# Optimization experiments

Measured on AMD Instinct MI355X. Metric: run time of the kernel, lower is better.

## Reference

```python
import jax, jax.numpy as jnp
import numpy as np

EMBED_DIM = 1024
NUM_HEADS = 16
HEAD_DIM = EMBED_DIM // NUM_HEADS
B, T = 4, 2048


def setup_inputs() -> dict:
    key = jax.random.key(0)
    ks = jax.random.split(key, 5)
    s = 1.0 / np.sqrt(EMBED_DIM)
    x = jax.random.normal(ks[0], (B, T, EMBED_DIM), dtype=jnp.float32)
    attention_mask = jnp.ones((B, 1, 1, T), dtype=jnp.int32)
    # torch Linear weights: qkv (3E, E), out (E, E); store transposed for x @ W
    W_qkv = jax.random.uniform(ks[1], (EMBED_DIM, 3 * EMBED_DIM), jnp.float32, -s, s)
    b_qkv = jax.random.uniform(ks[2], (3 * EMBED_DIM,), jnp.float32, -s, s)
    W_out = jax.random.uniform(ks[3], (EMBED_DIM, EMBED_DIM), jnp.float32, -s, s)
    b_out = jax.random.uniform(ks[4], (EMBED_DIM,), jnp.float32, -s, s)
    return {"x": x, "attention_mask": attention_mask,
            "W_qkv": W_qkv, "b_qkv": b_qkv, "W_out": W_out, "b_out": b_out}


def reference(x, attention_mask, W_qkv, b_qkv, W_out, b_out):
    Bq, Tq, E = x.shape
    qkv = x @ W_qkv + b_qkv                              # [B,T,3E]
    qkv = qkv.reshape(Bq, Tq, 3, NUM_HEADS, HEAD_DIM)
    qkv = jnp.transpose(qkv, (2, 0, 3, 1, 4))            # [3,B,H,T,d]
    q, k, v = qkv[0], qkv[1], qkv[2]
    scores = jnp.einsum('bhqd,bhkd->bhqk', q, k) / jnp.sqrt(
        jnp.asarray(HEAD_DIM, x.dtype))                  # [B,H,T,T]
    scores = jnp.where(attention_mask == 0, jnp.asarray(-jnp.inf, x.dtype), scores)
    attn = jax.nn.softmax(scores, axis=-1)
    ctx = jnp.einsum('bhqk,bhkd->bhqd', attn, v)         # [B,H,T,d]
    ctx = jnp.transpose(ctx, (0, 2, 1, 3)).reshape(Bq, Tq, E)
    return ctx @ W_out + b_out
```

## Files before the change

kernel.cpp:

```cpp
#include <hip/hip_runtime.h>
#include <hip/hip_bf16.h>
#include <stdint.h>


typedef __attribute__((ext_vector_type(8))) short short8;
typedef __attribute__((ext_vector_type(4))) float f32x4;
typedef __attribute__((ext_vector_type(16))) float f32x16;
typedef __attribute__((ext_vector_type(4))) unsigned short ushort4_t;
typedef __attribute__((ext_vector_type(8))) unsigned short ushort8_t;

#define SEQ 2048
#define EDIM 1024
#define QSCALE 0.18033688011112042f

__device__ __forceinline__ unsigned short f2bf(float x) {
  union { float f; uint32_t u; } v; v.f = x;
  uint32_t r = v.u + 0x7fffu + ((v.u >> 16) & 1u);
  return (unsigned short)(r >> 16);
}

__device__ __forceinline__ uint32_t cvtpk(float lo, float hi) {
  uint32_t r;
  asm("v_cvt_pk_bf16_f32 %0, %1, %2" : "=v"(r) : "v"(lo), "v"(hi));
  return r;
}

__device__ __forceinline__ float exp2_raw(float x) {
  float r;
  asm("v_exp_f32 %0, %1" : "=v"(r) : "v"(x));
  return r;
}

__device__ __forceinline__ void gload_lds16(const void* g, void* l) {
  typedef __attribute__((address_space(1))) const unsigned int gu32;
  typedef __attribute__((address_space(3))) unsigned int lu32;
  __builtin_amdgcn_global_load_lds((gu32*)g, (lu32*)l, 16, 0, 0);
}

__global__ void k_prep(const float* __restrict__ x,
                       unsigned short* __restrict__ xb,
                       const float* __restrict__ Wq,
                       unsigned short* __restrict__ wqt,
                       const float* __restrict__ Wo,
                       unsigned short* __restrict__ wot) {
  __shared__ float tile[32][33];
  const int id = blockIdx.x;
  if (id < 4096) {
    const int i = id * 256 + threadIdx.x;
    const float4* p = ((const float4*)x) + (size_t)i * 2;
    float4 a = p[0], b = p[1];
    ushort8_t v;
    v[0] = f2bf(a.x); v[1] = f2bf(a.y); v[2] = f2bf(a.z); v[3] = f2bf(a.w);
    v[4] = f2bf(b.x); v[5] = f2bf(b.y); v[6] = f2bf(b.z); v[7] = f2bf(b.w);
    ((ushort8_t*)xb)[i] = v;
    return;
  }
  const float* W;
  unsigned short* Wt;
  int N, bx, by;
  if (id < 7168) { W = Wq; Wt = wqt; N = 3072; bx = (id - 4096) % 96; by = (id - 4096) / 96; }
  else           { W = Wo; Wt = wot; N = 1024; bx = (id - 7168) % 32; by = (id - 7168) / 32; }
  const int K = 1024;
  const int c0 = bx * 32, r0 = by * 32;
  const int tx = threadIdx.x & 31, ty = threadIdx.x >> 5;
#pragma unroll
  for (int i = 0; i < 4; ++i) {
    int r = ty + i * 8;
    tile[r][tx] = W[(size_t)(r0 + r) * N + c0 + tx];
  }
  __syncthreads();
#pragma unroll
  for (int i = 0; i < 4; ++i) {
    int r = ty + i * 8;
    Wt[(size_t)(c0 + r) * K + r0 + tx] = f2bf(tile[tx][r]);
  }
}

template <int EPI, int NBX>
__global__ __launch_bounds__(256, 2) void k_gemm(
    const unsigned short* __restrict__ A, const unsigned short* __restrict__ Bt,
    const float* __restrict__ bias, unsigned short* __restrict__ Qo,
    unsigned short* __restrict__ Ko, unsigned short* __restrict__ VTo,
    float* __restrict__ Out) {
  __shared__ unsigned short As[128 * 32];
  __shared__ unsigned short Bs[128 * 32];
  const int tid = threadIdx.x;
  const int lane = tid & 63, wid = tid >> 6;
  const int wr = wid >> 1, wc = wid & 1;
  const int g = lane >> 4, r = lane & 15;
  const int lid = blockIdx.y * NBX + blockIdx.x;
  const int total = NBX * gridDim.y;
  const int id = (lid & 7) * (total >> 3) + (lid >> 3);
  const int m0 = (id / NBX) * 128, n0 = (id % NBX) * 128;

  f32x4 zero4 = {0.f, 0.f, 0.f, 0.f};
  f32x4 acc[4][4];
#pragma unroll
  for (int mi = 0; mi < 4; ++mi)
#pragma unroll
    for (int ni = 0; ni < 4; ++ni) acc[mi][ni] = zero4;

  for (int kt = 0; kt < 1024; kt += 32) {
#pragma unroll
    for (int i = 0; i < 2; ++i) {
      int seg = i * 256 + tid;
      int row = seg >> 2, sl = seg & 3;
      gload_lds16(A + (size_t)(m0 + row) * 1024 + kt + sl * 8,
                  (char*)As + (i * 256 + wid * 64) * 16);
      gload_lds16(Bt + (size_t)(n0 + row) * 1024 + kt + sl * 8,
                  (char*)Bs + (i * 256 + wid * 64) * 16);
    }
    __syncthreads();
    short8 af[4], bf[4];
#pragma unroll
    for (int mi = 0; mi < 4; ++mi)
      af[mi] = *(const short8*)&As[(wr * 64 + mi * 16 + r) * 32 + g * 8];
#pragma unroll
    for (int ni = 0; ni < 4; ++ni)
      bf[ni] = *(const short8*)&Bs[(wc * 64 + ni * 16 + r) * 32 + g * 8];
#pragma unroll
    for (int mi = 0; mi < 4; ++mi)
#pragma unroll
      for (int ni = 0; ni < 4; ++ni)
        acc[mi][ni] = __builtin_amdgcn_mfma_f32_16x16x32_bf16(
            af[mi], bf[ni], acc[mi][ni], 0, 0, 0);
    __syncthreads();
  }

#pragma unroll
  for (int mi = 0; mi < 4; ++mi) {
#pragma unroll
    for (int ni = 0; ni < 4; ++ni) {
      const int n = n0 + wc * 64 + ni * 16 + r;
      const float bv = bias[n];
      const int mbase = m0 + wr * 64 + mi * 16 + g * 4;
      if (EPI == 0) {
        const int sec = n >> 10, e = n & 1023, h = e >> 6, dd = e & 63;
        const int b = mbase >> 11, t = mbase & 2047;
        if (sec == 2) {
          ushort4_t pk;
#pragma unroll
          for (int j = 0; j < 4; ++j) pk[j] = f2bf(acc[mi][ni][j] + bv);
          *(ushort4_t*)&VTo[(((size_t)b * 16 + h) * 64 + dd) * 2048 + t] = pk;
        } else {
          unsigned short* dst = (sec == 0) ? Qo : Ko;
          const float scl = (sec == 0) ? QSCALE : 1.0f;
#pragma unroll
          for (int j = 0; j < 4; ++j)
            dst[(((size_t)b * 16 + h) * 2048 + t + j) * 64 + dd] =
                f2bf((acc[mi][ni][j] + bv) * scl);
        }
      } else {
#pragma unroll
        for (int j = 0; j < 4; ++j)
          Out[(size_t)(mbase + j) * 1024 + n] = acc[mi][ni][j] + bv;
      }
    }
  }
}

__global__ __launch_bounds__(256, 4) void k_attn(
    const unsigned short* __restrict__ Qg, const unsigned short* __restrict__ Kg,
    const unsigned short* __restrict__ VTg, const int* __restrict__ maskp,
    unsigned short* __restrict__ ctx) {
  __shared__ unsigned short Ks[3][64 * 64];
  __shared__ unsigned short Vs[3][64 * 64];
  const int tid = threadIdx.x, lane = tid & 63, wid = tid >> 6;
  const int q = lane & 31, hi = lane >> 5;
  const int id = blockIdx.x;
  const int slot = id >> 3;
  const int bh = (id & 7) * 8 + (slot >> 4);
  const int b = bh >> 4, h = bh & 15;
  const int q0 = (slot & 15) * 128 + wid * 32;
  const int qr = q0 + q;

  const unsigned short* Qb = Qg + (size_t)bh * SEQ * 64;
  const unsigned short* Kb = Kg + (size_t)bh * SEQ * 64;
  const unsigned short* Vb = VTg + (size_t)bh * 64 * SEQ;
  const int* mb = maskp + b * SEQ;

  const int r0_ = tid >> 3, sl0_ = (tid & 7) ^ (r0_ & 7);
  const int r1_ = (256 + tid) >> 3, sl1_ = ((256 + tid) & 7) ^ (r1_ & 7);
  const unsigned short* kp0 = Kb + r0_ * 64 + sl0_ * 8;
  const unsigned short* kp1 = Kb + r1_ * 64 + sl1_ * 8;
  const unsigned short* vp0 = Vb + (size_t)r0_ * SEQ + sl0_ * 8;
  const unsigned short* vp1 = Vb + (size_t)r1_ * SEQ + sl1_ * 8;
  char* kbase = (char*)Ks[0] + wid * 1024;
  char* vbase = (char*)Vs[0] + wid * 1024;

  auto STAGE = [&](int bo) {
    gload_lds16(kp0, kbase + bo);
    gload_lds16(kp1, kbase + bo + 4096);
    gload_lds16(vp0, vbase + bo);
    gload_lds16(vp1, vbase + bo + 4096);
    kp0 += 64 * 64; kp1 += 64 * 64;
    vp0 += 64; vp1 += 64;
  };

  short8 qf[4];
#pragma unroll
  for (int ds = 0; ds < 4; ++ds)
    qf[ds] = *(const short8*)&Qb[(size_t)qr * 64 + ds * 16 + hi * 8];

  short8 onesf;
#pragma unroll
  for (int j = 0; j < 8; ++j) onesf[j] = (short)0x3F80;

  f32x16 z16 = {0.f,0.f,0.f,0.f,0.f,0.f,0.f,0.f,0.f,0.f,0.f,0.f,0.f,0.f,0.f,0.f};
  f32x16 o0 = z16, o1 = z16;
  f32x16 osum = z16;
  short8 pfp[4];
#pragma unroll
  for (int j = 0; j < 4; ++j) pfp[j] = onesf;
  const int kb4 = hi * 4;

  STAGE(0);
  const int* mptr = mb + lane;
  int mv = mptr[0];
  mptr += 64;
  int cur = 0, nxt = 1, prv = 2;

  for (int t = 0; t < 32; ++t) {
    __syncthreads();
    int mvn = 1;
    if (t < 31) {
      STAGE(nxt * 8192);
      mvn = mptr[0];
      mptr += 64;
    }
    const unsigned long long bits = __ballot(mv != 0);
    mv = mvn;

    const char* KsB = (const char*)Ks[0] + cur * 8192;
    const char* VsP = (const char*)Vs[0] + prv * 8192;

    f32x16 c0 = z16, c1 = z16;
    __builtin_amdgcn_s_setprio(1);
#pragma unroll
    for (int ds = 0; ds < 4; ++ds) {
      const int sl = ds * 2 + hi;
      short8 ka0 = *(const short8*)(KsB + q * 128 + ((sl ^ (q & 7)) * 16));
      short8 ka1 = *(const short8*)(KsB + (32 + q) * 128 + ((sl ^ (q & 7)) * 16));
      c0 = __builtin_amdgcn_mfma_f32_32x32x16_bf16(ka0, qf[ds], c0, 0, 0, 0);
      c1 = __builtin_amdgcn_mfma_f32_32x32x16_bf16(ka1, qf[ds], c1, 0, 0, 0);
    }

    if (t > 0) {
#pragma unroll
      for (int ks = 0; ks < 4; ++ks) {
        const int sl = ks * 2 + hi;
        short8 va0 = *(const short8*)(VsP + q * 128 + ((sl ^ (q & 7)) * 16));
        short8 va1 = *(const short8*)(VsP + (32 + q) * 128 + ((sl ^ (q & 7)) * 16));
        o0 = __builtin_amdgcn_mfma_f32_32x32x16_bf16(va0, pfp[ks], o0, 0, 0, 0);
        o1 = __builtin_amdgcn_mfma_f32_32x32x16_bf16(va1, pfp[ks], o1, 0, 0, 0);
        osum = __builtin_amdgcn_mfma_f32_32x32x16_bf16(onesf, pfp[ks], osum,
                                                       0, 0, 0);
      }
    }
    __builtin_amdgcn_s_setprio(0);

#pragma unroll
    for (int i = 0; i < 16; ++i) {
      c0[i] = exp2_raw(c0[i]);
      c1[i] = exp2_raw(c1[i]);
    }
    if (bits != ~0ull) {
#pragma unroll
      for (int i = 0; i < 16; ++i) {
        const int k0 = (i & 3) + 8 * (i >> 2) + kb4;
        if (!((bits >> k0) & 1)) c0[i] = 0.f;
        if (!((bits >> (k0 + 32)) & 1)) c1[i] = 0.f;
      }
    }

#pragma unroll
    for (int sub = 0; sub < 2; ++sub) {
      uint32_t w[8];
#pragma unroll
      for (int j = 0; j < 8; ++j)
        w[j] = sub ? cvtpk(c1[2 * j], c1[2 * j + 1])
                   : cvtpk(c0[2 * j], c0[2 * j + 1]);
      asm("v_permlane32_swap_b32 %0, %1" : "+v"(w[0]), "+v"(w[2]));
      asm("v_permlane32_swap_b32 %0, %1" : "+v"(w[1]), "+v"(w[3]));
      asm("v_permlane32_swap_b32 %0, %1" : "+v"(w[4]), "+v"(w[6]));
      asm("v_permlane32_swap_b32 %0, %1" : "+v"(w[5]), "+v"(w[7]));
      union { uint32_t u[4]; short8 s; } ua, ub;
      ua.u[0] = w[0]; ua.u[1] = w[1]; ua.u[2] = w[2]; ua.u[3] = w[3];
      ub.u[0] = w[4]; ub.u[1] = w[5]; ub.u[2] = w[6]; ub.u[3] = w[7];
      pfp[sub * 2] = ua.s;
      pfp[sub * 2 + 1] = ub.s;
    }

    prv = cur; cur = nxt; nxt = (nxt == 2) ? 0 : nxt + 1;
  }

  {
    const char* VsP = (const char*)Vs[0] + prv * 8192;
    __builtin_amdgcn_s_setprio(1);
#pragma unroll
    for (int ks = 0; ks < 4; ++ks) {
      const int sl = ks * 2 + hi;
      short8 va0 = *(const short8*)(VsP + q * 128 + ((sl ^ (q & 7)) * 16));
      short8 va1 = *(const short8*)(VsP + (32 + q) * 128 + ((sl ^ (q & 7)) * 16));
      o0 = __builtin_amdgcn_mfma_f32_32x32x16_bf16(va0, pfp[ks], o0, 0, 0, 0);
      o1 = __builtin_amdgcn_mfma_f32_32x32x16_bf16(va1, pfp[ks], o1, 0, 0, 0);
      osum = __builtin_amdgcn_mfma_f32_32x32x16_bf16(onesf, pfp[ks], osum,
                                                     0, 0, 0);
    }
    __builtin_amdgcn_s_setprio(0);
  }

  const float inv = 1.f / osum[0];
#pragma unroll
  for (int ns = 0; ns < 2; ++ns) {
#pragma unroll
    for (int g_ = 0; g_ < 4; ++g_) {
      ushort4_t v4;
#pragma unroll
      for (int e = 0; e < 4; ++e) {
        const float val = (ns ? o1[g_ * 4 + e] : o0[g_ * 4 + e]) * inv;
        v4[e] = f2bf(val);
      }
      *(ushort4_t*)&ctx[((size_t)b * SEQ + qr) * 1024 + h * 64 + ns * 32 +
                        g_ * 8 + hi * 4] = v4;
    }
  }
}

extern "C" void kernel_launch(void* const* d_in, const int* in_sizes, int n_in,
                              void* d_out, int out_size, void* d_ws,
                              size_t ws_size, hipStream_t stream) {
  const float* x = (const float*)d_in[0];
  const int* mask = (const int*)d_in[1];
  const float* Wqkv = (const float*)d_in[2];
  const float* bqkv = (const float*)d_in[3];
  const float* Wout = (const float*)d_in[4];
  const float* bout = (const float*)d_in[5];
  float* out = (float*)d_out;

  unsigned short* ws = (unsigned short*)d_ws;
  unsigned short* xb = ws;
  unsigned short* wqt = ws + 8388608;
  unsigned short* wot = ws + 11534336;
  unsigned short* Q = ws + 12582912;
  unsigned short* K = ws + 20971520;
  unsigned short* VT = ws + 29360128;
  unsigned short* ctx = xb;

  k_prep<<<8192, 256, 0, stream>>>(x, xb, Wqkv, wqt, Wout, wot);
  k_gemm<0, 24><<<dim3(24, 64), 256, 0, stream>>>(xb, wqt, bqkv, Q, K, VT,
                                                  nullptr);
  k_attn<<<1024, 256, 0, stream>>>(Q, K, VT, mask, ctx);
  k_gemm<1, 8><<<dim3(8, 64), 256, 0, stream>>>(ctx, wot, bout, nullptr,
                                                nullptr, nullptr, out);
}
```

Baseline: 202.5 us.

## Split attention KV tiles across wave pairs and reduce partial outputs in LDS

Each attention block now covers 64 queries with four waves arranged as two query groups times two key halves, so the grid doubles to 2048 blocks. Each wave computes scores for 32 of the 64 keys in a tile and accumulates a partial PV product and row sum. The partials are combined through LDS at the end. The software pipeline drops from three buffers with a one-step deferred PV to two buffers with the PV done in the same step, which cuts LDS use and lengthens the dependency chain inside each iteration. This trades more K/V tile loads per query and an extra reduction for higher parallelism and occupancy.

After: 251.1 us. 1.24x slower.

```diff
diff --git a/kernel.cpp b/kernel.cpp
--- a/kernel.cpp
+++ b/kernel.cpp
@@ -163,15 +163,16 @@
     const unsigned short* __restrict__ Qg, const unsigned short* __restrict__ Kg,
     const unsigned short* __restrict__ VTg, const int* __restrict__ maskp,
     unsigned short* __restrict__ ctx) {
-  __shared__ unsigned short Ks[3][64 * 64];
-  __shared__ unsigned short Vs[3][64 * 64];
+  __shared__ unsigned short Ks[2][64 * 64];
+  __shared__ unsigned short Vs[2][64 * 64];
   const int tid = threadIdx.x, lane = tid & 63, wid = tid >> 6;
+  const int wq = wid >> 1, wk = wid & 1;
   const int q = lane & 31, hi = lane >> 5;
   const int id = blockIdx.x;
   const int slot = id >> 3;
-  const int bh = (id & 7) * 8 + (slot >> 4);
+  const int bh = (id & 7) * 8 + (slot >> 5);
   const int b = bh >> 4, h = bh & 15;
-  const int q0 = (slot & 15) * 128 + wid * 32;
+  const int q0 = (slot & 31) * 64 + wq * 32;
   const int qr = q0 + q;
 
   const unsigned short* Qb = Qg + (size_t)bh * SEQ * 64;
@@ -188,7 +189,8 @@
   char* kbase = (char*)Ks[0] + wid * 1024;
   char* vbase = (char*)Vs[0] + wid * 1024;
 
-  auto STAGE = [&](int bo) {
+  auto STAGE = [&](int buf) {
+    const int bo = buf * 8192;
     gload_lds16(kp0, kbase + bo);
     gload_lds16(kp1, kbase + bo + 4096);
     gload_lds16(vp0, vbase + bo);
@@ -209,77 +211,54 @@
   f32x16 z16 = {0.f,0.f,0.f,0.f,0.f,0.f,0.f,0.f,0.f,0.f,0.f,0.f,0.f,0.f,0.f,0.f};
   f32x16 o0 = z16, o1 = z16;
   f32x16 osum = z16;
-  short8 pfp[4];
-#pragma unroll
-  for (int j = 0; j < 4; ++j) pfp[j] = onesf;
   const int kb4 = hi * 4;
 
   STAGE(0);
   const int* mptr = mb + lane;
   int mv = mptr[0];
   mptr += 64;
-  int cur = 0, nxt = 1, prv = 2;
 
   for (int t = 0; t < 32; ++t) {
+    const int cur = t & 1;
     __syncthreads();
     int mvn = 1;
     if (t < 31) {
-      STAGE(nxt * 8192);
+      STAGE(cur ^ 1);
       mvn = mptr[0];
       mptr += 64;
     }
     const unsigned long long bits = __ballot(mv != 0);
     mv = mvn;
 
-    const char* KsB = (const char*)Ks[0] + cur * 8192;
-    const char* VsP = (const char*)Vs[0] + prv * 8192;
-
-    f32x16 c0 = z16, c1 = z16;
+    const char* KsB = (const char*)Ks[cur];
+    const char* VsB = (const char*)Vs[cur];
+
+    f32x16 c0 = z16;
     __builtin_amdgcn_s_setprio(1);
 #pragma unroll
     for (int ds = 0; ds < 4; ++ds) {
       const int sl = ds * 2 + hi;
-      short8 ka0 = *(const short8*)(KsB + q * 128 + ((sl ^ (q & 7)) * 16));
-      short8 ka1 = *(const short8*)(KsB + (32 + q) * 128 + ((sl ^ (q & 7)) * 16));
-      c0 = __builtin_amdgcn_mfma_f32_32x32x16_bf16(ka0, qf[ds], c0, 0, 0, 0);
-      c1 = __builtin_amdgcn_mfma_f32_32x32x16_bf16(ka1, qf[ds], c1, 0, 0, 0);
-    }
-
-    if (t > 0) {
-#pragma unroll
-      for (int ks = 0; ks < 4; ++ks) {
-        const int sl = ks * 2 + hi;
-        short8 va0 = *(const short8*)(VsP + q * 128 + ((sl ^ (q & 7)) * 16));
-        short8 va1 = *(const short8*)(VsP + (32 + q) * 128 + ((sl ^ (q & 7)) * 16));
-        o0 = __builtin_amdgcn_mfma_f32_32x32x16_bf16(va0, pfp[ks], o0, 0, 0, 0);
-        o1 = __builtin_amdgcn_mfma_f32_32x32x16_bf16(va1, pfp[ks], o1, 0, 0, 0);
-        osum = __builtin_amdgcn_mfma_f32_32x32x16_bf16(onesf, pfp[ks], osum,
-                                                       0, 0, 0);
+      short8 ka = *(const short8*)(KsB + (wk * 32 + q) * 128 +
+                                   ((sl ^ (q & 7)) * 16));
+      c0 = __builtin_amdgcn_mfma_f32_32x32x16_bf16(ka, qf[ds], c0, 0, 0, 0);
+    }
+    __builtin_amdgcn_s_setprio(0);
+
+#pragma unroll
+    for (int i = 0; i < 16; ++i) c0[i] = exp2_raw(c0[i]);
+    if (bits != ~0ull) {
+#pragma unroll
+      for (int i = 0; i < 16; ++i) {
+        const int k0 = wk * 32 + (i & 3) + 8 * (i >> 2) + kb4;
+        if (!((bits >> k0) & 1)) c0[i] = 0.f;
       }
     }
-    __builtin_amdgcn_s_setprio(0);
-
-#pragma unroll
-    for (int i = 0; i < 16; ++i) {
-      c0[i] = exp2_raw(c0[i]);
-      c1[i] = exp2_raw(c1[i]);
-    }
-    if (bits != ~0ull) {
-#pragma unroll
-      for (int i = 0; i < 16; ++i) {
-        const int k0 = (i & 3) + 8 * (i >> 2) + kb4;
-        if (!((bits >> k0) & 1)) c0[i] = 0.f;
-        if (!((bits >> (k0 + 32)) & 1)) c1[i] = 0.f;
-      }
-    }
-
-#pragma unroll
-    for (int sub = 0; sub < 2; ++sub) {
+
+    short8 pf[2];
+    {
       uint32_t w[8];
 #pragma unroll
-      for (int j = 0; j < 8; ++j)
-        w[j] = sub ? cvtpk(c1[2 * j], c1[2 * j + 1])
-                   : cvtpk(c0[2 * j], c0[2 * j + 1]);
+      for (int j = 0; j < 8; ++j) w[j] = cvtpk(c0[2 * j], c0[2 * j + 1]);
       asm("v_permlane32_swap_b32 %0, %1" : "+v"(w[0]), "+v"(w[2]));
       asm("v_permlane32_swap_b32 %0, %1" : "+v"(w[1]), "+v"(w[3]));
       asm("v_permlane32_swap_b32 %0, %1" : "+v"(w[4]), "+v"(w[6]));
@@ -287,42 +266,53 @@
       union { uint32_t u[4]; short8 s; } ua, ub;
       ua.u[0] = w[0]; ua.u[1] = w[1]; ua.u[2] = w[2]; ua.u[3] = w[3];
       ub.u[0] = w[4]; ub.u[1] = w[5]; ub.u[2] = w[6]; ub.u[3] = w[7];
-      pfp[sub * 2] = ua.s;
-      pfp[sub * 2 + 1] = ub.s;
-    }
-
-    prv = cur; cur = nxt; nxt = (nxt == 2) ? 0 : nxt + 1;
-  }
-
-  {
-    const char* VsP = (const char*)Vs[0] + prv * 8192;
+      pf[0] = ua.s;
+      pf[1] = ub.s;
+    }
+
     __builtin_amdgcn_s_setprio(1);
 #pragma unroll
-    for (int ks = 0; ks < 4; ++ks) {
-      const int sl = ks * 2 + hi;
-      short8 va0 = *(const short8*)(VsP + q * 128 + ((sl ^ (q & 7)) * 16));
-      short8 va1 = *(const short8*)(VsP + (32 + q) * 128 + ((sl ^ (q & 7)) * 16));
-      o0 = __builtin_amdgcn_mfma_f32_32x32x16_bf16(va0, pfp[ks], o0, 0, 0, 0);
-      o1 = __builtin_amdgcn_mfma_f32_32x32x16_bf16(va1, pfp[ks], o1, 0, 0, 0);
-      osum = __builtin_amdgcn_mfma_f32_32x32x16_bf16(onesf, pfp[ks], osum,
+    for (int ks = 0; ks < 2; ++ks) {
+      const int sl = wk * 4 + ks * 2 + hi;
+      short8 va0 = *(const short8*)(VsB + q * 128 + ((sl ^ (q & 7)) * 16));
+      short8 va1 = *(const short8*)(VsB + (32 + q) * 128 + ((sl ^ (q & 7)) * 16));
+      o0 = __builtin_amdgcn_mfma_f32_32x32x16_bf16(va0, pf[ks], o0, 0, 0, 0);
+      o1 = __builtin_amdgcn_mfma_f32_32x32x16_bf16(va1, pf[ks], o1, 0, 0, 0);
+      osum = __builtin_amdgcn_mfma_f32_32x32x16_bf16(onesf, pf[ks], osum,
                                                      0, 0, 0);
     }
     __builtin_amdgcn_s_setprio(0);
   }
 
-  const float inv = 1.f / osum[0];
-#pragma unroll
-  for (int ns = 0; ns < 2; ++ns) {
-#pragma unroll
-    for (int g_ = 0; g_ < 4; ++g_) {
-      ushort4_t v4;
-#pragma unroll
-      for (int e = 0; e < 4; ++e) {
-        const float val = (ns ? o1[g_ * 4 + e] : o0[g_ * 4 + e]) * inv;
-        v4[e] = f2bf(val);
+  __syncthreads();
+  float* red = (wq == 0) ? (float*)&Ks[0][0] : (float*)&Vs[0][0];
+  if (wk == 1) {
+#pragma unroll
+    for (int i = 0; i < 16; ++i) red[i * 64 + lane] = o0[i];
+#pragma unroll
+    for (int i = 0; i < 16; ++i) red[(16 + i) * 64 + lane] = o1[i];
+    red[32 * 64 + lane] = osum[0];
+  }
+  __syncthreads();
+  if (wk == 0) {
+#pragma unroll
+    for (int i = 0; i < 16; ++i) o0[i] += red[i * 64 + lane];
+#pragma unroll
+    for (int i = 0; i < 16; ++i) o1[i] += red[(16 + i) * 64 + lane];
+    const float inv = 1.f / (osum[0] + red[32 * 64 + lane]);
+#pragma unroll
+    for (int ns = 0; ns < 2; ++ns) {
+#pragma unroll
+      for (int g_ = 0; g_ < 4; ++g_) {
+        ushort4_t v4;
+#pragma unroll
+        for (int e = 0; e < 4; ++e) {
+          const float val = (ns ? o1[g_ * 4 + e] : o0[g_ * 4 + e]) * inv;
+          v4[e] = f2bf(val);
+        }
+        *(ushort4_t*)&ctx[((size_t)b * SEQ + qr) * 1024 + h * 64 + ns * 32 +
+                          g_ * 8 + hi * 4] = v4;
       }
-      *(ushort4_t*)&ctx[((size_t)b * SEQ + qr) * 1024 + h * 64 + ns * 32 +
-                        g_ * 8 + hi * 4] = v4;
     }
   }
 }
@@ -350,7 +340,7 @@
   k_prep<<<8192, 256, 0, stream>>>(x, xb, Wqkv, wqt, Wout, wot);
   k_gemm<0, 24><<<dim3(24, 64), 256, 0, stream>>>(xb, wqt, bqkv, Q, K, VT,
                                                   nullptr);
-  k_attn<<<1024, 256, 0, stream>>>(Q, K, VT, mask, ctx);
+  k_attn<<<2048, 256, 0, stream>>>(Q, K, VT, mask, ctx);
   k_gemm<1, 8><<<dim3(8, 64), 256, 0, stream>>>(ctx, wot, bout, nullptr,
                                                 nullptr, nullptr, out);
 }
```
